# Kernel optimization log

Hardware: AMD Instinct MI355X
Metric: run time of the kernel (lower is better)

## Reference

```python
import jax, jax.numpy as jnp
import numpy as np

EMBED_DIM = 1024
NUM_HEADS = 16
HEAD_DIM = EMBED_DIM // NUM_HEADS  # 64, used only for score scaling
B, S = 4, 2048


def setup_inputs() -> dict:
    key = jax.random.key(0)
    k1, k2, k3, k4 = jax.random.split(key, 4)
    rotation_params = jax.random.normal(k1, (3 * EMBED_DIM * EMBED_DIM,), dtype=jnp.float32) * 0.02
    entangle_params = jax.random.normal(k2, (EMBED_DIM * EMBED_DIM,), dtype=jnp.float32) * 0.02
    inputs = jax.random.normal(k3, (B, S, EMBED_DIM), dtype=jnp.float32)
    gate_w = jax.random.normal(k4, (EMBED_DIM, EMBED_DIM), dtype=jnp.float32) * 0.02
    return {"rotation_params": rotation_params, "entangle_params": entangle_params,
            "inputs": inputs, "gate_w": gate_w}


def reference(rotation_params, entangle_params, inputs, gate_w):
    E = EMBED_DIM
    w_qkv = rotation_params.reshape(3 * E, E)   # nn.Linear weight layout (out, in)
    w_out = entangle_params.reshape(E, E)
    # qkv projection: x @ W^T, then chunk into q, k, v along last dim
    qkv = jnp.einsum('bse,fe->bsf', inputs, w_qkv)  # (B, S, 3E)
    q, k, v = jnp.split(qkv, 3, axis=-1)
    # NOTE: original code does NOT split into heads; attention over full E,
    # scaled by sqrt(head_dim).
    q = q * (1.0 / np.sqrt(HEAD_DIM)).astype(np.float32)
    scores = jnp.einsum('bqe,bke->bqk', q, k)       # (B, S, S)
    attn = jax.nn.softmax(scores, axis=-1)
    attn_out = jnp.einsum('bqk,bke->bqe', attn, v)  # (B, S, E)
    out = jnp.einsum('bse,fe->bsf', attn_out, w_out)
    gate = jax.nn.sigmoid(jnp.einsum('bse,fe->bsf', out, gate_w))
    return gate * out
```

## Files before the change

### kernel.cpp

```cpp
#include <hip/hip_runtime.h>
#include <math.h>

#define EMB 1024
#define NB 4
#define SQ 2048
#define TOK (NB*SQ)

typedef __attribute__((ext_vector_type(8))) short bhalf8;
typedef __attribute__((ext_vector_type(4))) float f32x4;

__device__ __forceinline__ unsigned short f32_to_bf16(float f) {
    unsigned int u = __float_as_uint(f);
    u += 0x7FFFu + ((u >> 16) & 1u);
    return (unsigned short)(u >> 16);
}
__device__ __forceinline__ float bf16_to_f32(unsigned short h) {
    return __uint_as_float(((unsigned int)h) << 16);
}
__device__ __forceinline__ unsigned short f32_to_f16(float f) {
    union { _Float16 h; unsigned short u; } c; c.h = (_Float16)f; return c.u;
}
__device__ __forceinline__ float f16_to_f32(unsigned short u) {
    union { _Float16 h; unsigned short u; } c; c.u = u; return (float)c.h;
}

__global__ __launch_bounds__(256) void convert_all_kernel(
    const float* __restrict__ x,  unsigned short* __restrict__ x_bf,
    const float* __restrict__ rot, const float* __restrict__ ent,
    const float* __restrict__ gw, unsigned short* __restrict__ w_bf) {
    const int EE4 = EMB * EMB / 4;
    const float* src;
    unsigned short* dst;
    float scale = 1.0f;
    int j;
    if (blockIdx.x < TOK*EMB/4/256) {
        src = x; dst = x_bf; j = blockIdx.x * 256 + threadIdx.x;
        float4 v = ((const float4*)src)[j];
        ushort4 o = { f32_to_bf16(v.x), f32_to_bf16(v.y), f32_to_bf16(v.z), f32_to_bf16(v.w) };
        ((ushort4*)dst)[j] = o;
        return;
    }
    const int i = (blockIdx.x - TOK*EMB/4/256) * 256 + threadIdx.x;
    j = i; dst = w_bf;
    if (i < 3 * EE4) {
        src = rot;
        if (i < EE4) scale = 0.125f;
    } else if (i < 4 * EE4) { src = ent; j = i - 3 * EE4; }
    else                    { src = gw;  j = i - 4 * EE4; }
    float4 v = ((const float4*)src)[j];
    ushort4 o;
    o.x = f32_to_bf16(v.x * scale);
    o.y = f32_to_bf16(v.y * scale);
    o.z = f32_to_bf16(v.z * scale);
    o.w = f32_to_bf16(v.w * scale);
    ((ushort4*)dst)[i] = o;
}

__device__ __forceinline__ void async_load16(const unsigned short* gp, unsigned short* lp) {
    __builtin_amdgcn_global_load_lds(
        (const __attribute__((address_space(1))) unsigned int*)gp,
        (__attribute__((address_space(3))) unsigned int*)lp,
        16, 0, 0);
}

template <int MODE>
__global__ __launch_bounds__(256) void gemm_nt_128(
    const unsigned short* __restrict__ A,
    const unsigned short* __restrict__ B,
    void* __restrict__ C,
    const unsigned short* __restrict__ Obf,
    float* __restrict__ Fout,
    int M, int N, int K, int lda, int ldb, int ldc,
    long sA, long sB, long sC)
{
    __shared__ __align__(16) unsigned short As[128*64];
    __shared__ __align__(16) unsigned short Bs[128*64];

    const int bz = blockIdx.z;
    const unsigned short* Ab = A + (long)bz * sA;
    const unsigned short* Bb = B + (long)bz * sB;
    const int bm = blockIdx.x * 128;
    const int bn = blockIdx.y * 128;
    const int t = threadIdx.x;
    const int w = t >> 6;
    const int l = t & 63;
    const int srow8 = l >> 3;
    const int scol  = (((l & 7) ^ ((l >> 3) & 7)) * 8);

    f32x4 zero = {0.f, 0.f, 0.f, 0.f};
    f32x4 acc[4][4];
    #pragma unroll
    for (int i = 0; i < 4; ++i)
        #pragma unroll
        for (int j = 0; j < 4; ++j) acc[i][j] = zero;

    const int wm = (w >> 1) * 64;
    const int wn = (w & 1) * 64;
    const int fr = l & 15;
    const int kqs0 = ((((l >> 4)    ) ^ (l & 7)) * 8);
    const int kqs1 = (((4 + (l >> 4)) ^ (l & 7)) * 8);

    const int nkt = K >> 6;
    for (int kt = 0; kt < nkt; ++kt) {
        const int k0 = kt << 6;
        __syncthreads();
        #pragma unroll
        for (int r = 0; r < 4; ++r) {
            const int rr = (r*4 + w) * 8 + srow8;
            async_load16(Ab + (long)(bm + rr) * lda + (k0 + scol), As + (r*4 + w) * 512);
            async_load16(Bb + (long)(bn + rr) * ldb + (k0 + scol), Bs + (r*4 + w) * 512);
        }
        __syncthreads();

        #pragma unroll
        for (int h = 0; h < 2; ++h) {
            const int kq = h ? kqs1 : kqs0;
            bhalf8 af[4], bfr[4];
            #pragma unroll
            for (int mi = 0; mi < 4; ++mi)
                af[mi] = *(const bhalf8*)(As + (wm + mi*16 + fr) * 64 + kq);
            #pragma unroll
            for (int ni = 0; ni < 4; ++ni)
                bfr[ni] = *(const bhalf8*)(Bs + (wn + ni*16 + fr) * 64 + kq);
            #pragma unroll
            for (int mi = 0; mi < 4; ++mi)
                #pragma unroll
                for (int ni = 0; ni < 4; ++ni)
                    acc[mi][ni] = __builtin_amdgcn_mfma_f32_16x16x32_bf16(
                        af[mi], bfr[ni], acc[mi][ni], 0, 0, 0);
        }
    }

    const int crow = (l >> 4) * 4;
    const int ccol = l & 15;
    #pragma unroll
    for (int mi = 0; mi < 4; ++mi) {
        #pragma unroll
        for (int ni = 0; ni < 4; ++ni) {
            #pragma unroll
            for (int r = 0; r < 4; ++r) {
                const int gr = bm + wm + mi*16 + crow + r;
                const int gc = bn + wn + ni*16 + ccol;
                const float v = acc[mi][ni][r];
                const long idx = (long)gr * ldc + gc;
                if (MODE == 0) {
                    ((unsigned short*)C)[(long)bz*sC + idx] = f32_to_bf16(v);
                } else if (MODE == 1) {
                    ((unsigned short*)C)[(long)bz*sC + idx] = f32_to_f16(v);
                } else {
                    const float o = bf16_to_f32(Obf[idx]);
                    const float g = 1.0f / (1.0f + __expf(-v));
                    Fout[idx] = g * o;
                }
            }
        }
    }
}


#define BARF() asm volatile("s_barrier" ::: "memory")
#define VMC6() asm volatile("s_waitcnt vmcnt(6)" ::: "memory")
#define VMC0() asm volatile("s_waitcnt vmcnt(0)" ::: "memory")

#define STAGE_A(buf, half, kofs) do { \
    async_load16(aG0 + (half)*aH + (kofs), &As[buf][(half)*8192 +        w*512]); \
    async_load16(aG1 + (half)*aH + (kofs), &As[buf][(half)*8192 + 4096 + w*512]); \
} while (0)
#define STAGE_B(buf, half, kofs) do { \
    async_load16(bG0 + (half)*bH + (kofs), &Bs[buf][(half)*8192 +        w*512]); \
    async_load16(bG1 + (half)*bH + (kofs), &Bs[buf][(half)*8192 + 4096 + w*512]); \
} while (0)

#define READ_A(p) do { \
    af[0][0] = *(const bhalf8*)(aRd + ((p)*2    )*1024 + kqs0); \
    af[0][1] = *(const bhalf8*)(aRd + ((p)*2    )*1024 + kqs1); \
    af[1][0] = *(const bhalf8*)(aRd + ((p)*2 + 1)*1024 + kqs0); \
    af[1][1] = *(const bhalf8*)(aRd + ((p)*2 + 1)*1024 + kqs1); \
} while (0)

#define READ_B() do { \
    _Pragma("unroll") \
    for (int ni_ = 0; ni_ < 4; ++ni_) { \
        bfv[ni_][0] = *(const bhalf8*)(bRd + ni_*1024 + kqs0); \
        bfv[ni_][1] = *(const bhalf8*)(bRd + ni_*1024 + kqs1); \
    } \
} while (0)

#define MFMA16(p) do { \
    __builtin_amdgcn_s_setprio(1); \
    _Pragma("unroll") \
    for (int h_ = 0; h_ < 2; ++h_) { \
        _Pragma("unroll") \
        for (int mi_ = 0; mi_ < 2; ++mi_) { \
            _Pragma("unroll") \
            for (int ni_ = 0; ni_ < 4; ++ni_) \
                acc[(p)*2 + mi_][ni_] = __builtin_amdgcn_mfma_f32_16x16x32_bf16( \
                    af[mi_][h_], bfv[ni_][h_], acc[(p)*2 + mi_][ni_], 0, 0, 0); \
        } \
    } \
    __builtin_amdgcn_s_setprio(0); \
} while (0)

template <int MODE>
__global__ __launch_bounds__(512, 2) void gemm_nt_8p(
    const unsigned short* __restrict__ A,
    const unsigned short* __restrict__ B,
    void* __restrict__ C,
    const unsigned short* __restrict__ Obf,
    float* __restrict__ Fout,
    int M, int N, int K, int lda, int ldb, int ldc,
    long sA, long sB, long sC)
{
    __shared__ __align__(16) unsigned short As[2][16384];
    __shared__ __align__(16) unsigned short Bs[2][16384];

    const int bz = blockIdx.z;
    const unsigned short* Ab = A + (long)bz * sA;
    const unsigned short* Bb = B + (long)bz * sB;
    const int bm = blockIdx.x * 256;
    const int bn = blockIdx.y * 256;
    const int t = threadIdx.x;
    const int w = t >> 6;
    const int l = t & 63;

    const int srow = l >> 3;
    const int scol = (((l & 7) ^ (l >> 3)) * 8);

    const int fr = l & 15;
    const int kqs0 = ((((l >> 4)    ) ^ (l & 7)) * 8);
    const int kqs1 = (((4 + (l >> 4)) ^ (l & 7)) * 8);

    const int wm = (w >> 2) * 128;
    const int wn = (w & 3) * 64;

    f32x4 acc[8][4];
    f32x4 zero = {0.f, 0.f, 0.f, 0.f};
    #pragma unroll
    for (int i = 0; i < 8; ++i)
        #pragma unroll
        for (int j = 0; j < 4; ++j) acc[i][j] = zero;

    const unsigned short* aG0 = Ab + (long)(bm + (    w)*8 + srow) * lda + scol;
    const unsigned short* aG1 = Ab + (long)(bm + (8 + w)*8 + srow) * lda + scol;
    const unsigned short* bG0 = Bb + (long)(bn + (    w)*8 + srow) * ldb + scol;
    const unsigned short* bG1 = Bb + (long)(bn + (8 + w)*8 + srow) * ldb + scol;
    const long aH = (long)128 * lda;
    const long bH = (long)128 * ldb;

    const int nkt = K >> 6;

    STAGE_A(0, 0, 0);  STAGE_A(0, 1, 0);
    STAGE_B(0, 0, 0);  STAGE_B(0, 1, 0);
    STAGE_B(1, 0, 64); STAGE_B(1, 1, 64);
    STAGE_A(1, 0, 64);
    VMC6();
    BARF();

    for (int kt = 0; kt < nkt; ++kt) {
        const int cur = kt & 1, nxt = cur ^ 1;
        const unsigned short* aRd = &As[cur][(wm + fr) * 64];
        const unsigned short* bRd = &Bs[cur][(wn + fr) * 64];
        const bool s1 = (kt + 1 < nkt);
        const bool s2 = (kt + 2 < nkt);
        const int k1 = (kt + 1) << 6;
        const int k2 = (kt + 2) << 6;

        bhalf8 bfv[4][2], af[2][2];

        if (s1) STAGE_A(nxt, 1, k1);
        READ_B();
        READ_A(0);
        MFMA16(0);
        BARF();

        if (s2) STAGE_B(cur, 0, k2);
        READ_A(1);
        MFMA16(1);

        if (s2) STAGE_B(cur, 1, k2);
        READ_A(2);
        MFMA16(2);
        BARF();

        if (s2) STAGE_A(cur, 0, k2);
        READ_A(3);
        MFMA16(3);
        if (s2) VMC6(); else VMC0();
        BARF();
    }

    const int crow = (l >> 4) * 4;
    const int ccol = l & 15;
    #pragma unroll
    for (int mi = 0; mi < 8; ++mi) {
        #pragma unroll
        for (int ni = 0; ni < 4; ++ni) {
            #pragma unroll
            for (int r = 0; r < 4; ++r) {
                const int gr = bm + wm + mi*16 + crow + r;
                const int gc = bn + wn + ni*16 + ccol;
                const float v = acc[mi][ni][r];
                const long idx = (long)gr * ldc + gc;
                if (MODE == 0) {
                    ((unsigned short*)C)[(long)bz*sC + idx] = f32_to_bf16(v);
                } else if (MODE == 1) {
                    ((unsigned short*)C)[(long)bz*sC + idx] = f32_to_f16(v);
                } else {
                    const float o = bf16_to_f32(Obf[idx]);
                    const float g = 1.0f / (1.0f + __expf(-v));
                    Fout[idx] = g * o;
                }
            }
        }
    }
}

#undef BARF
#undef VMC6
#undef VMC0
#undef STAGE_A
#undef STAGE_B
#undef READ_A
#undef READ_B
#undef MFMA16

__global__ __launch_bounds__(256) void softmax_kernel(const unsigned short* __restrict__ sc,
                                                      unsigned short* __restrict__ attn) {
    const long row = blockIdx.x;
    const unsigned short* p = sc + row * SQ;
    unsigned short* q = attn + row * SQ;
    const int t = threadIdx.x;
    const int w = t >> 6, l = t & 63;
    union { bhalf8 v; unsigned short u[8]; } in;
    in.v = ((const bhalf8*)p)[t];
    float f[8];
    float m = -1e30f;
    #pragma unroll
    for (int j = 0; j < 8; ++j) { f[j] = f16_to_f32(in.u[j]); m = fmaxf(m, f[j]); }
    #pragma unroll
    for (int off = 32; off; off >>= 1) m = fmaxf(m, __shfl_xor(m, off));
    __shared__ float smax[4], ssum[4];
    if (l == 0) smax[w] = m;
    __syncthreads();
    m = fmaxf(fmaxf(smax[0], smax[1]), fmaxf(smax[2], smax[3]));
    float s = 0.f;
    #pragma unroll
    for (int j = 0; j < 8; ++j) { f[j] = __expf(f[j] - m); s += f[j]; }
    #pragma unroll
    for (int off = 32; off; off >>= 1) s += __shfl_xor(s, off);
    if (l == 0) ssum[w] = s;
    __syncthreads();
    const float inv = 1.0f / (ssum[0] + ssum[1] + ssum[2] + ssum[3]);
    union { bhalf8 v; unsigned short u[8]; } o;
    #pragma unroll
    for (int j = 0; j < 8; ++j) o.u[j] = f32_to_bf16(f[j] * inv);
    ((bhalf8*)q)[t] = o.v;
}

__global__ void transpose_v(const unsigned short* __restrict__ qkv,
                            unsigned short* __restrict__ vT) {
    __shared__ unsigned short tile[32][33];
    const int b = blockIdx.z;
    const unsigned short* v = qkv + (long)b * SQ * (3*EMB) + 2*EMB;
    const int e = blockIdx.x * 32 + threadIdx.x;
    const int s = blockIdx.y * 32 + threadIdx.y;
    tile[threadIdx.y][threadIdx.x] = v[(long)s * (3*EMB) + e];
    __syncthreads();
    const int so = blockIdx.y * 32 + threadIdx.x;
    const int eo = blockIdx.x * 32 + threadIdx.y;
    vT[(long)b * EMB * SQ + (long)eo * SQ + so] = tile[threadIdx.x][threadIdx.y];
}

extern "C" void kernel_launch(void* const* d_in, const int* in_sizes, int n_in,
                              void* d_out, int out_size, void* d_ws, size_t ws_size,
                              hipStream_t stream) {
    const float* rot = (const float*)d_in[0];
    const float* ent = (const float*)d_in[1];
    const float* x   = (const float*)d_in[2];
    const float* gw  = (const float*)d_in[3];
    float* outp = (float*)d_out;
    char* ws = (char*)d_ws;

    size_t off = 0;
    unsigned short* x_bf    = (unsigned short*)(ws + off); off += (size_t)TOK*EMB*2;
    unsigned short* wqkv_bf = (unsigned short*)(ws + off); off += (size_t)3*EMB*EMB*2;
    unsigned short* wout_bf = (unsigned short*)(ws + off); off += (size_t)EMB*EMB*2;
    unsigned short* gate_bf = (unsigned short*)(ws + off); off += (size_t)EMB*EMB*2;
    unsigned short* qkv_bf  = (unsigned short*)(ws + off); off += (size_t)TOK*3*EMB*2;
    unsigned short* vT_bf   = (unsigned short*)(ws + off); off += (size_t)NB*EMB*SQ*2;
    unsigned short* sc_f16  = (unsigned short*)(ws + off); off += (size_t)NB*SQ*SQ*2;
    unsigned short* attn_bf = qkv_bf;
    unsigned short* ao_bf   = x_bf;
    unsigned short* out_bf  = qkv_bf + (size_t)NB*SQ*SQ;

    convert_all_kernel<<<dim3(TOK*EMB/4/256 + 5*EMB*EMB/4/256), dim3(256), 0, stream>>>(
        x, x_bf, rot, ent, gw, wqkv_bf);

    gemm_nt_8p<0><<<dim3(TOK/256, 3*EMB/256, 1), dim3(512), 0, stream>>>(
        x_bf, wqkv_bf, qkv_bf, nullptr, nullptr,
        TOK, 3*EMB, EMB, EMB, EMB, 3*EMB, 0, 0, 0);

    transpose_v<<<dim3(EMB/32, SQ/32, NB), dim3(32, 32), 0, stream>>>(qkv_bf, vT_bf);

    gemm_nt_8p<1><<<dim3(SQ/256, SQ/256, NB), dim3(512), 0, stream>>>(
        qkv_bf, qkv_bf + EMB, sc_f16, nullptr, nullptr,
        SQ, SQ, EMB, 3*EMB, 3*EMB, SQ,
        (long)SQ*3*EMB, (long)SQ*3*EMB, (long)SQ*SQ);

    softmax_kernel<<<dim3(NB*SQ), dim3(256), 0, stream>>>(sc_f16, attn_bf);

    gemm_nt_128<0><<<dim3(SQ/128, EMB/128, NB), dim3(256), 0, stream>>>(
        attn_bf, vT_bf, ao_bf, nullptr, nullptr,
        SQ, EMB, SQ, SQ, SQ, EMB,
        (long)SQ*SQ, (long)EMB*SQ, (long)SQ*EMB);

    gemm_nt_128<0><<<dim3(TOK/128, EMB/128, 1), dim3(256), 0, stream>>>(
        ao_bf, wout_bf, out_bf, nullptr, nullptr,
        TOK, EMB, EMB, EMB, EMB, EMB, 0, 0, 0);

    gemm_nt_128<2><<<dim3(TOK/128, EMB/128, 1), dim3(256), 0, stream>>>(
        out_bf, gate_bf, nullptr, out_bf, outp,
        TOK, EMB, EMB, EMB, EMB, EMB, 0, 0, 0);
}
```

Baseline: 329.6 us.

## Software-pipeline LDS fragment reads in the 256x256 GEMM and use the 128-tile kernel for QKV

Rewrites the 8-wave 256x256 GEMM main loop so LDS fragment reads for the next MFMA group are issued before the current group runs. The B fragments alternate between two register sets across an unrolled pair of k-tiles. The goal is to hide LDS read latency behind MFMA work, at the cost of more registers and a changed barrier placement. The QKV projection is also switched to the 128x128 GEMM kernel, and only the scores GEMM uses the new pipelined kernel.

```diff
diff --git a/kernel.cpp b/kernel.cpp
--- a/kernel.cpp
+++ b/kernel.cpp
@@ -171,38 +171,68 @@
     async_load16(bG1 + (half)*bH + (kofs), &Bs[buf][(half)*8192 + 4096 + w*512]); \
 } while (0)
 
-#define READ_A(p) do { \
-    af[0][0] = *(const bhalf8*)(aRd + ((p)*2    )*1024 + kqs0); \
-    af[0][1] = *(const bhalf8*)(aRd + ((p)*2    )*1024 + kqs1); \
-    af[1][0] = *(const bhalf8*)(aRd + ((p)*2 + 1)*1024 + kqs0); \
-    af[1][1] = *(const bhalf8*)(aRd + ((p)*2 + 1)*1024 + kqs1); \
-} while (0)
-
-#define READ_B() do { \
+#define RD_A(dst, base, p) do { \
+    dst[0][0] = *(const bhalf8*)((base) + ((p)*2    )*1024 + kqs0); \
+    dst[0][1] = *(const bhalf8*)((base) + ((p)*2    )*1024 + kqs1); \
+    dst[1][0] = *(const bhalf8*)((base) + ((p)*2 + 1)*1024 + kqs0); \
+    dst[1][1] = *(const bhalf8*)((base) + ((p)*2 + 1)*1024 + kqs1); \
+} while (0)
+
+#define RD_B(dst, base) do { \
     _Pragma("unroll") \
     for (int ni_ = 0; ni_ < 4; ++ni_) { \
-        bfv[ni_][0] = *(const bhalf8*)(bRd + ni_*1024 + kqs0); \
-        bfv[ni_][1] = *(const bhalf8*)(bRd + ni_*1024 + kqs1); \
+        dst[ni_][0] = *(const bhalf8*)((base) + ni_*1024 + kqs0); \
+        dst[ni_][1] = *(const bhalf8*)((base) + ni_*1024 + kqs1); \
     } \
 } while (0)
 
-#define MFMA16(p) do { \
+#define MFMA8(p, Aset, Bset) do { \
     __builtin_amdgcn_s_setprio(1); \
     _Pragma("unroll") \
-    for (int h_ = 0; h_ < 2; ++h_) { \
+    for (int h_ = 0; h_ < 2; ++h_) \
         _Pragma("unroll") \
-        for (int mi_ = 0; mi_ < 2; ++mi_) { \
+        for (int mi_ = 0; mi_ < 2; ++mi_) \
             _Pragma("unroll") \
             for (int ni_ = 0; ni_ < 4; ++ni_) \
                 acc[(p)*2 + mi_][ni_] = __builtin_amdgcn_mfma_f32_16x16x32_bf16( \
-                    af[mi_][h_], bfv[ni_][h_], acc[(p)*2 + mi_][ni_], 0, 0, 0); \
-        } \
-    } \
+                    Aset[mi_][h_], Bset[ni_][h_], acc[(p)*2 + mi_][ni_], 0, 0, 0); \
     __builtin_amdgcn_s_setprio(0); \
 } while (0)
 
+#define TILE_V3(kt, CUR, Bc, Bn) do { \
+    const int cur_ = (CUR); const int nxt_ = cur_ ^ 1; \
+    const bool s1 = (kt) + 1 < nkt; \
+    const bool s2 = (kt) + 2 < nkt; \
+    const int k1 = ((kt) + 1) << 6; \
+    const int k2 = ((kt) + 2) << 6; \
+    const unsigned short* aRd  = &As[cur_][(wm + fr) * 64]; \
+    const unsigned short* aRdN = &As[nxt_][(wm + fr) * 64]; \
+    const unsigned short* bRdN = &Bs[nxt_][(wn + fr) * 64]; \
+     \
+    RD_A(Ab, aRd, 1); \
+    if (s1) STAGE_A(nxt_, 1, k1); \
+    BARF(); \
+    MFMA8(0, Aa, Bc); \
+     \
+    RD_A(Aa, aRd, 2); \
+    if (s2) STAGE_B(cur_, 0, k2); \
+    BARF(); \
+    MFMA8(1, Ab, Bc); \
+     \
+    RD_A(Aa2, aRd, 3); \
+    if (s2) STAGE_B(cur_, 1, k2); \
+    BARF(); \
+    MFMA8(2, Aa, Bc); \
+     \
+     \
+    if (s2) { STAGE_A(cur_, 0, k2); VMC6(); } else { VMC0(); } \
+    BARF(); \
+    if (s1) { RD_A(Aa, aRdN, 0); RD_B(Bn, bRdN); } \
+    MFMA8(3, Aa2, Bc); \
+} while (0)
+
 template <int MODE>
-__global__ __launch_bounds__(512, 2) void gemm_nt_8p(
+__global__ __launch_bounds__(512, 2) void gemm_nt_v3(
     const unsigned short* __restrict__ A,
     const unsigned short* __restrict__ B,
     void* __restrict__ C,
@@ -215,8 +245,8 @@
     __shared__ __align__(16) unsigned short Bs[2][16384];
 
     const int bz = blockIdx.z;
-    const unsigned short* Ab = A + (long)bz * sA;
-    const unsigned short* Bb = B + (long)bz * sB;
+    const unsigned short* Ab_ = A + (long)bz * sA;
+    const unsigned short* Bb_ = B + (long)bz * sB;
     const int bm = blockIdx.x * 256;
     const int bn = blockIdx.y * 256;
     const int t = threadIdx.x;
@@ -240,14 +270,17 @@
         #pragma unroll
         for (int j = 0; j < 4; ++j) acc[i][j] = zero;
 
-    const unsigned short* aG0 = Ab + (long)(bm + (    w)*8 + srow) * lda + scol;
-    const unsigned short* aG1 = Ab + (long)(bm + (8 + w)*8 + srow) * lda + scol;
-    const unsigned short* bG0 = Bb + (long)(bn + (    w)*8 + srow) * ldb + scol;
-    const unsigned short* bG1 = Bb + (long)(bn + (8 + w)*8 + srow) * ldb + scol;
+    const unsigned short* aG0 = Ab_ + (long)(bm + (    w)*8 + srow) * lda + scol;
+    const unsigned short* aG1 = Ab_ + (long)(bm + (8 + w)*8 + srow) * lda + scol;
+    const unsigned short* bG0 = Bb_ + (long)(bn + (    w)*8 + srow) * ldb + scol;
+    const unsigned short* bG1 = Bb_ + (long)(bn + (8 + w)*8 + srow) * ldb + scol;
     const long aH = (long)128 * lda;
     const long bH = (long)128 * ldb;
 
     const int nkt = K >> 6;
+
+    bhalf8 Aa[2][2], Ab[2][2], Aa2[2][2];
+    bhalf8 B0[4][2], B1[4][2];
 
     STAGE_A(0, 0, 0);  STAGE_A(0, 1, 0);
     STAGE_B(0, 0, 0);  STAGE_B(0, 1, 0);
@@ -255,38 +288,16 @@
     STAGE_A(1, 0, 64);
     VMC6();
     BARF();
-
-    for (int kt = 0; kt < nkt; ++kt) {
-        const int cur = kt & 1, nxt = cur ^ 1;
-        const unsigned short* aRd = &As[cur][(wm + fr) * 64];
-        const unsigned short* bRd = &Bs[cur][(wn + fr) * 64];
-        const bool s1 = (kt + 1 < nkt);
-        const bool s2 = (kt + 2 < nkt);
-        const int k1 = (kt + 1) << 6;
-        const int k2 = (kt + 2) << 6;
-
-        bhalf8 bfv[4][2], af[2][2];
-
-        if (s1) STAGE_A(nxt, 1, k1);
-        READ_B();
-        READ_A(0);
-        MFMA16(0);
-        BARF();
-
-        if (s2) STAGE_B(cur, 0, k2);
-        READ_A(1);
-        MFMA16(1);
-
-        if (s2) STAGE_B(cur, 1, k2);
-        READ_A(2);
-        MFMA16(2);
-        BARF();
-
-        if (s2) STAGE_A(cur, 0, k2);
-        READ_A(3);
-        MFMA16(3);
-        if (s2) VMC6(); else VMC0();
-        BARF();
+    {
+        const unsigned short* aRd0 = &As[0][(wm + fr) * 64];
+        const unsigned short* bRd0 = &Bs[0][(wn + fr) * 64];
+        RD_A(Aa, aRd0, 0);
+        RD_B(B0, bRd0);
+    }
+
+    for (int kt = 0; kt < nkt; kt += 2) {
+        TILE_V3(kt,     0, B0, B1);
+        TILE_V3(kt + 1, 1, B1, B0);
     }
 
     const int crow = (l >> 4) * 4;
@@ -320,9 +331,10 @@
 #undef VMC0
 #undef STAGE_A
 #undef STAGE_B
-#undef READ_A
-#undef READ_B
-#undef MFMA16
+#undef RD_A
+#undef RD_B
+#undef MFMA8
+#undef TILE_V3
 
 __global__ __launch_bounds__(256) void softmax_kernel(const unsigned short* __restrict__ sc,
                                                       unsigned short* __restrict__ attn) {
@@ -396,13 +408,13 @@
     convert_all_kernel<<<dim3(TOK*EMB/4/256 + 5*EMB*EMB/4/256), dim3(256), 0, stream>>>(
         x, x_bf, rot, ent, gw, wqkv_bf);
 
-    gemm_nt_8p<0><<<dim3(TOK/256, 3*EMB/256, 1), dim3(512), 0, stream>>>(
+    gemm_nt_128<0><<<dim3(TOK/128, 3*EMB/128, 1), dim3(256), 0, stream>>>(
         x_bf, wqkv_bf, qkv_bf, nullptr, nullptr,
         TOK, 3*EMB, EMB, EMB, EMB, 3*EMB, 0, 0, 0);
 
     transpose_v<<<dim3(EMB/32, SQ/32, NB), dim3(32, 32), 0, stream>>>(qkv_bf, vT_bf);
 
-    gemm_nt_8p<1><<<dim3(SQ/256, SQ/256, NB), dim3(512), 0, stream>>>(
+    gemm_nt_v3<1><<<dim3(SQ/256, SQ/256, NB), dim3(512), 0, stream>>>(
         qkv_bf, qkv_bf + EMB, sc_f16, nullptr, nullptr,
         SQ, SQ, EMB, 3*EMB, 3*EMB, SQ,
         (long)SQ*3*EMB, (long)SQ*3*EMB, (long)SQ*SQ);
```

After: 331.0 us. Within noise of the previous version (+0.4%).
